# Optimization experiments

Measured on AMD Instinct MI355X. Metric: run time of the kernel, lower is better.

The kernel has to match this reference:

```python
import jax, jax.numpy as jnp
import numpy as np

NUM_CLASSES = 1000  # label vocabulary size (matches fill_max for label)
B = 16384
D_IN = 1024   # image_embedding
D_OUT = 256   # projection_dim


def setup_inputs() -> dict:
    key = jax.random.key(0)
    k = jax.random.split(key, 6)
    x = jax.random.normal(k[0], (B, D_IN), dtype=jnp.float32)
    label = jax.random.randint(k[1], (B,), 0, NUM_CLASSES, dtype=jnp.int64)
    scale = 1.0 / np.sqrt(D_IN)
    W1_w = jax.random.normal(k[2], (D_OUT, D_IN), dtype=jnp.float32) * scale
    W1_b = jax.random.normal(k[3], (D_OUT,), dtype=jnp.float32) * scale
    W2_w = jax.random.normal(k[4], (D_OUT, D_IN), dtype=jnp.float32) * scale
    W2_b = jax.random.normal(k[5], (D_OUT,), dtype=jnp.float32) * scale
    return {"x": x, "label": label, "W1_w": W1_w, "W1_b": W1_b,
            "W2_w": W2_w, "W2_b": W2_b}


def reference(x, label, W1_w, W1_b, W2_w, W2_b):
    # Leave-one-group-out mean, vectorized via segment sums.
    # Original: for each i, mean of x[label != label_i] (detached); zeros if none.
    b = x.shape[0]
    xd = jax.lax.stop_gradient(x)  # .detach() in the torch code
    label_sum = jax.ops.segment_sum(xd, label, num_segments=NUM_CLASSES)          # [C, D_IN]
    label_cnt = jax.ops.segment_sum(jnp.ones((b,), dtype=x.dtype), label,
                                    num_segments=NUM_CLASSES)                     # [C]
    total_sum = xd.sum(axis=0)                                                    # [D_IN]
    other_sum = total_sum[None, :] - label_sum[label]                             # [B, D_IN]
    other_cnt = jnp.asarray(b, x.dtype) - label_cnt[label]                        # [B]
    calculate_mean = jnp.where(other_cnt[:, None] > 0,
                               other_sum / jnp.maximum(other_cnt, 1)[:, None],
                               jnp.zeros((), x.dtype))                            # [B, D_IN]
    # W1(x) + W2(calculate_mean)  (torch Linear: y = x @ W.T + b)
    return x @ W1_w.T + W1_b + calculate_mean @ W2_w.T + W2_b
```

## Files before the change

### kernel.cpp

```cpp
#include <hip/hip_runtime.h>

constexpr int B      = 16384;
constexpr int D_IN   = 1024;
constexpr int D_OUT  = 256;
constexpr int NCLS   = 1000;

constexpr size_t OFF_XB  = 0;
constexpr size_t OFF_WB  = OFF_XB + (size_t)B * D_IN * 2;
constexpr size_t OFF_Y1  = OFF_WB + (size_t)512 * D_IN * 2;
constexpr size_t OFF_V   = OFF_Y1 + (size_t)B * D_OUT * 4;
constexpr size_t OFF_U   = OFF_V  + (size_t)1024 * D_OUT * 4;
constexpr size_t OFF_CNT = OFF_U  + 4096;

typedef short bf16x8 __attribute__((ext_vector_type(8)));
typedef float f32x4  __attribute__((ext_vector_type(4)));

__device__ __forceinline__ unsigned short f2bf(float f) {
    unsigned int u = __float_as_uint(f);
    return (unsigned short)((u + 0x7FFFu + ((u >> 16) & 1u)) >> 16);
}

__device__ __forceinline__ void cvt8(const float4& a, const float4& b, unsigned short* dst) {
    union { unsigned short u[8]; bf16x8 v; } r;
    r.u[0] = f2bf(a.x); r.u[1] = f2bf(a.y); r.u[2] = f2bf(a.z); r.u[3] = f2bf(a.w);
    r.u[4] = f2bf(b.x); r.u[5] = f2bf(b.y); r.u[6] = f2bf(b.z); r.u[7] = f2bf(b.w);
    *(bf16x8*)dst = r.v;
}

__device__ __forceinline__ void async16(const unsigned short* g, unsigned short* l) {
    __builtin_amdgcn_global_load_lds(
        (const __attribute__((address_space(1))) void*)g,
        (__attribute__((address_space(3))) void*)l,
        16, 0, 0);
}

constexpr int XCVT_BLKS = 8192;
constexpr int WCVT_BLKS = 256;
constexpr int VZ_BLKS   = 64;
__global__ __launch_bounds__(256)
void prep_kernel(const float* __restrict__ x,
                 const float* __restrict__ W1, const float* __restrict__ W2,
                 const int* __restrict__ label,
                 unsigned short* __restrict__ xb, unsigned short* __restrict__ Wb,
                 float* __restrict__ V, float* __restrict__ U, int* __restrict__ cnt) {
    const int blk = blockIdx.x, tid = threadIdx.x;
    if (blk < XCVT_BLKS) {
        size_t lin = (size_t)blk * 256 + tid;
        const float* src = x + lin * 8;
        float4 a = *(const float4*)src;
        float4 b = *(const float4*)(src + 4);
        cvt8(a, b, xb + lin * 8);
    } else if (blk < XCVT_BLKS + WCVT_BLKS) {
        int lin = (blk - XCVT_BLKS) * 256 + tid;
        int i = lin * 8;
        const float* src = (i < D_OUT * D_IN) ? (W1 + i) : (W2 + (i - D_OUT * D_IN));
        float4 a = *(const float4*)src;
        float4 b = *(const float4*)(src + 4);
        cvt8(a, b, Wb + i);
    } else if (blk < XCVT_BLKS + WCVT_BLKS + VZ_BLKS) {
        int lb = blk - (XCVT_BLKS + WCVT_BLKS);
        int base = (lb * 256 + tid) * 16;
#pragma unroll
        for (int q = 0; q < 4; ++q)
            *(float4*)(V + base + q * 4) = float4{0.f, 0.f, 0.f, 0.f};
        if (lb == 0 && tid < 64)
            *(float4*)(U + tid * 4) = float4{0.f, 0.f, 0.f, 0.f};
    } else {
        __shared__ int h[1024];
#pragma unroll
        for (int q = 0; q < 4; ++q) h[q * 256 + tid] = 0;
        __syncthreads();
        for (int r = 0; r < 64; ++r)
            atomicAdd(&h[label[r * 256 + tid]], 1);
        __syncthreads();
#pragma unroll
        for (int q = 0; q < 4; ++q) cnt[q * 256 + tid] = h[q * 256 + tid];
    }
}

__global__ __launch_bounds__(256)
void gemm_kernel(const unsigned short* __restrict__ xb,
                 const unsigned short* __restrict__ Wb,
                 const int* __restrict__ label,
                 float* __restrict__ y1,
                 float* __restrict__ V, float* __restrict__ U) {
    __shared__ unsigned short As[2][128][32];
    __shared__ unsigned short Bs[2][64][32];

    const int tid  = threadIdx.x;
    const int bid  = blockIdx.x;
    const int xcd   = bid & 7;
    const int local = bid >> 3;
    const int bx = xcd * 16 + (local & 15);
    const int by = local >> 4;
    const int bm = bx * 128;
    const int bn = by * 64;

    const int wave = tid >> 6, lane = tid & 63;
    const int quad = lane >> 4, l16 = lane & 15;
    const int wm = (wave >> 1) * 64;
    const int wn = (wave & 1) * 32;

    const unsigned short* aps[4];
#pragma unroll
    for (int rr = 0; rr < 4; ++rr) {
        int dd = rr * 256 + tid;
        int h = dd >> 9, r = (dd >> 2) & 127, c = dd & 3;
        aps[rr] = xb + (size_t)(bm + r) * D_IN + h * 32 + c * 8;
    }
    const unsigned short* bps[2];
#pragma unroll
    for (int rr = 0; rr < 2; ++rr) {
        int dd = rr * 256 + tid;
        int h = dd >> 8, r = (dd >> 2) & 63, c = dd & 3;
        bps[rr] = Wb + (size_t)(bn + r) * D_IN + h * 32 + c * 8;
    }

    f32x4 acc[4][2] = {};

    for (int k0 = 0; k0 < D_IN; k0 += 64) {
        __syncthreads();
#pragma unroll
        for (int rr = 0; rr < 4; ++rr)
            async16(aps[rr] + k0, &As[0][0][0] + rr * 2048 + wave * 512);
#pragma unroll
        for (int rr = 0; rr < 2; ++rr)
            async16(bps[rr] + k0, &Bs[0][0][0] + rr * 2048 + wave * 512);
        __syncthreads();

#pragma unroll
        for (int ks = 0; ks < 2; ++ks) {
            bf16x8 af[4], bfr[2];
#pragma unroll
            for (int i = 0; i < 4; ++i)
                af[i] = *(const bf16x8*)&As[ks][wm + i * 16 + l16][quad * 8];
#pragma unroll
            for (int j = 0; j < 2; ++j)
                bfr[j] = *(const bf16x8*)&Bs[ks][wn + j * 16 + l16][quad * 8];
#pragma unroll
            for (int i = 0; i < 4; ++i)
#pragma unroll
                for (int j = 0; j < 2; ++j)
                    acc[i][j] = __builtin_amdgcn_mfma_f32_16x16x32_bf16(af[i], bfr[j], acc[i][j], 0, 0, 0);
        }
    }

    if (by < 4) {
#pragma unroll
        for (int j = 0; j < 2; ++j) {
            const int n = bn + wn + j * 16 + l16;
#pragma unroll
            for (int i = 0; i < 4; ++i)
#pragma unroll
                for (int r = 0; r < 4; ++r) {
                    const int m = bm + wm + i * 16 + quad * 4 + r;
                    y1[(size_t)m * D_OUT + n] = acc[i][j][r];
                }
        }
    } else {
        int lab[4][4];
#pragma unroll
        for (int i = 0; i < 4; ++i)
#pragma unroll
            for (int r = 0; r < 4; ++r)
                lab[i][r] = label[bm + wm + i * 16 + quad * 4 + r] * D_OUT;

        const int nb = bn - 256;
#pragma unroll
        for (int j = 0; j < 2; ++j) {
            const int n = nb + wn + j * 16 + l16;
            float cs = 0.f;
#pragma unroll
            for (int i = 0; i < 4; ++i)
#pragma unroll
                for (int r = 0; r < 4; ++r) {
                    float v = acc[i][j][r];
                    cs += v;
                    atomicAdd(&V[lab[i][r] + n], v);
                }
            cs += __shfl_xor(cs, 16);
            cs += __shfl_xor(cs, 32);
            if (quad == 0) atomicAdd(&U[n], cs);
        }
    }
}

__global__ __launch_bounds__(256)
void epi_kernel(const float* __restrict__ y1, const float* __restrict__ V,
                const float* __restrict__ U,
                const float* __restrict__ b1, const float* __restrict__ b2,
                const int* __restrict__ cnt, const int* __restrict__ label,
                float* __restrict__ out) {
    const int tid = threadIdx.x;
    const int row = blockIdx.x * 64 + (tid >> 2);
    const int lab = label[row];
    const float inv = 1.0f / (float)(B - cnt[lab]);
    const float* yp = y1 + (size_t)row * D_OUT;
    const float* vp = V  + (size_t)lab * D_OUT;
    float* op = out + (size_t)row * D_OUT;
    const int c0 = (tid & 3) * 4;
#pragma unroll
    for (int it = 0; it < 16; ++it) {
        const int c = c0 + it * 16;
        float4 y = *(const float4*)(yp + c);
        float4 v = *(const float4*)(vp + c);
        float4 u = *(const float4*)(U + c);
        float4 a1 = *(const float4*)(b1 + c);
        float4 a2 = *(const float4*)(b2 + c);
        float4 o;
        o.x = y.x + a1.x + a2.x + (u.x - v.x) * inv;
        o.y = y.y + a1.y + a2.y + (u.y - v.y) * inv;
        o.z = y.z + a1.z + a2.z + (u.z - v.z) * inv;
        o.w = y.w + a1.w + a2.w + (u.w - v.w) * inv;
        *(float4*)(op + c) = o;
    }
}

extern "C" void kernel_launch(void* const* d_in, const int* in_sizes, int n_in,
                              void* d_out, int out_size, void* d_ws, size_t ws_size,
                              hipStream_t stream) {
    const float* x    = (const float*)d_in[0];
    const int*   lab  = (const int*)d_in[1];
    const float* W1_w = (const float*)d_in[2];
    const float* W1_b = (const float*)d_in[3];
    const float* W2_w = (const float*)d_in[4];
    const float* W2_b = (const float*)d_in[5];
    float* out = (float*)d_out;

    char* ws = (char*)d_ws;
    unsigned short* xb = (unsigned short*)(ws + OFF_XB);
    unsigned short* Wb = (unsigned short*)(ws + OFF_WB);
    float* y1 = (float*)(ws + OFF_Y1);
    float* V  = (float*)(ws + OFF_V);
    float* U  = (float*)(ws + OFF_U);
    int*   cnt = (int*)(ws + OFF_CNT);

    prep_kernel<<<XCVT_BLKS + WCVT_BLKS + VZ_BLKS + 1, 256, 0, stream>>>(
        x, W1_w, W2_w, lab, xb, Wb, V, U, cnt);
    gemm_kernel<<<1024, 256, 0, stream>>>(xb, Wb, lab, y1, V, U);
    epi_kernel<<<B / 64, 256, 0, stream>>>(y1, V, U, W1_b, W2_b, cnt, lab, out);
}
```

Baseline: 183.5 us.

## Enlarge GEMM tile to 128x128 with XOR-swizzled LDS and batch prep work

The GEMM block tile grows from 128x64 to 128x128, so each wave computes 64x64 and the grid halves to 512 blocks. This raises the MFMA-to-load ratio and cuts redundant reads of the x tiles. Shared memory is now a single 64-wide K slab per row with an XOR swizzle, intended to avoid LDS bank conflicts. The prep kernel converts 16 elements per thread, moves the label histogram to block 0 so it starts early, and batches its label loads. Costs are higher register use per thread (16 accumulators) and fewer blocks for 256 CUs, which may lower occupancy.

```diff
diff --git a/kernel.cpp b/kernel.cpp
--- a/kernel.cpp
+++ b/kernel.cpp
@@ -34,8 +34,8 @@
         16, 0, 0);
 }
 
-constexpr int XCVT_BLKS = 8192;
-constexpr int WCVT_BLKS = 256;
+constexpr int XCVT_BLKS = 4096;
+constexpr int WCVT_BLKS = 128;
 constexpr int VZ_BLKS   = 64;
 __global__ __launch_bounds__(256)
 void prep_kernel(const float* __restrict__ x,
@@ -44,37 +44,48 @@
                  unsigned short* __restrict__ xb, unsigned short* __restrict__ Wb,
                  float* __restrict__ V, float* __restrict__ U, int* __restrict__ cnt) {
     const int blk = blockIdx.x, tid = threadIdx.x;
-    if (blk < XCVT_BLKS) {
-        size_t lin = (size_t)blk * 256 + tid;
-        const float* src = x + lin * 8;
-        float4 a = *(const float4*)src;
-        float4 b = *(const float4*)(src + 4);
-        cvt8(a, b, xb + lin * 8);
-    } else if (blk < XCVT_BLKS + WCVT_BLKS) {
-        int lin = (blk - XCVT_BLKS) * 256 + tid;
-        int i = lin * 8;
+    if (blk == 0) {
+        __shared__ int h[1024];
+#pragma unroll
+        for (int q = 0; q < 4; ++q) h[q * 256 + tid] = 0;
+        __syncthreads();
+        for (int base = 0; base < 64; base += 16) {
+            int lv[16];
+#pragma unroll
+            for (int u = 0; u < 16; ++u) lv[u] = label[(base + u) * 256 + tid];
+#pragma unroll
+            for (int u = 0; u < 16; ++u) atomicAdd(&h[lv[u]], 1);
+        }
+        __syncthreads();
+#pragma unroll
+        for (int q = 0; q < 4; ++q) cnt[q * 256 + tid] = h[q * 256 + tid];
+    } else if (blk <= XCVT_BLKS) {
+        size_t lin = (size_t)(blk - 1) * 256 + tid;
+        const float* src = x + lin * 16;
+        float4 a0 = *(const float4*)(src);
+        float4 a1 = *(const float4*)(src + 4);
+        float4 a2 = *(const float4*)(src + 8);
+        float4 a3 = *(const float4*)(src + 12);
+        cvt8(a0, a1, xb + lin * 16);
+        cvt8(a2, a3, xb + lin * 16 + 8);
+    } else if (blk <= XCVT_BLKS + WCVT_BLKS) {
+        int lin = (blk - 1 - XCVT_BLKS) * 256 + tid;
+        int i = lin * 16;
         const float* src = (i < D_OUT * D_IN) ? (W1 + i) : (W2 + (i - D_OUT * D_IN));
-        float4 a = *(const float4*)src;
-        float4 b = *(const float4*)(src + 4);
-        cvt8(a, b, Wb + i);
-    } else if (blk < XCVT_BLKS + WCVT_BLKS + VZ_BLKS) {
-        int lb = blk - (XCVT_BLKS + WCVT_BLKS);
+        float4 a0 = *(const float4*)(src);
+        float4 a1 = *(const float4*)(src + 4);
+        float4 a2 = *(const float4*)(src + 8);
+        float4 a3 = *(const float4*)(src + 12);
+        cvt8(a0, a1, Wb + i);
+        cvt8(a2, a3, Wb + i + 8);
+    } else {
+        int lb = blk - 1 - XCVT_BLKS - WCVT_BLKS;
         int base = (lb * 256 + tid) * 16;
 #pragma unroll
         for (int q = 0; q < 4; ++q)
             *(float4*)(V + base + q * 4) = float4{0.f, 0.f, 0.f, 0.f};
         if (lb == 0 && tid < 64)
             *(float4*)(U + tid * 4) = float4{0.f, 0.f, 0.f, 0.f};
-    } else {
-        __shared__ int h[1024];
-#pragma unroll
-        for (int q = 0; q < 4; ++q) h[q * 256 + tid] = 0;
-        __syncthreads();
-        for (int r = 0; r < 64; ++r)
-            atomicAdd(&h[label[r * 256 + tid]], 1);
-        __syncthreads();
-#pragma unroll
-        for (int q = 0; q < 4; ++q) cnt[q * 256 + tid] = h[q * 256 + tid];
     }
 }
 
@@ -84,8 +95,8 @@
                  const int* __restrict__ label,
                  float* __restrict__ y1,
                  float* __restrict__ V, float* __restrict__ U) {
-    __shared__ unsigned short As[2][128][32];
-    __shared__ unsigned short Bs[2][64][32];
+    __shared__ unsigned short As[128][64];
+    __shared__ unsigned short Bs[128][64];
 
     const int tid  = threadIdx.x;
     const int bid  = blockIdx.x;
@@ -94,60 +105,58 @@
     const int bx = xcd * 16 + (local & 15);
     const int by = local >> 4;
     const int bm = bx * 128;
-    const int bn = by * 64;
+    const int bn = by * 128;
 
     const int wave = tid >> 6, lane = tid & 63;
     const int quad = lane >> 4, l16 = lane & 15;
     const int wm = (wave >> 1) * 64;
-    const int wn = (wave & 1) * 32;
+    const int wn = (wave & 1) * 64;
+    const int sx = l16 & 7;
 
     const unsigned short* aps[4];
+    const unsigned short* bps[4];
 #pragma unroll
     for (int rr = 0; rr < 4; ++rr) {
         int dd = rr * 256 + tid;
-        int h = dd >> 9, r = (dd >> 2) & 127, c = dd & 3;
-        aps[rr] = xb + (size_t)(bm + r) * D_IN + h * 32 + c * 8;
-    }
-    const unsigned short* bps[2];
-#pragma unroll
-    for (int rr = 0; rr < 2; ++rr) {
-        int dd = rr * 256 + tid;
-        int h = dd >> 8, r = (dd >> 2) & 63, c = dd & 3;
-        bps[rr] = Wb + (size_t)(bn + r) * D_IN + h * 32 + c * 8;
-    }
-
-    f32x4 acc[4][2] = {};
+        int r = dd >> 3, sl = dd & 7;
+        int sc = sl ^ (r & 7);
+        aps[rr] = xb + (size_t)(bm + r) * D_IN + sc * 8;
+        bps[rr] = Wb + (size_t)(bn + r) * D_IN + sc * 8;
+    }
+
+    f32x4 acc[4][4] = {};
 
     for (int k0 = 0; k0 < D_IN; k0 += 64) {
         __syncthreads();
 #pragma unroll
         for (int rr = 0; rr < 4; ++rr)
-            async16(aps[rr] + k0, &As[0][0][0] + rr * 2048 + wave * 512);
-#pragma unroll
-        for (int rr = 0; rr < 2; ++rr)
-            async16(bps[rr] + k0, &Bs[0][0][0] + rr * 2048 + wave * 512);
+            async16(aps[rr] + k0, &As[0][0] + rr * 2048 + wave * 512);
+#pragma unroll
+        for (int rr = 0; rr < 4; ++rr)
+            async16(bps[rr] + k0, &Bs[0][0] + rr * 2048 + wave * 512);
         __syncthreads();
 
 #pragma unroll
         for (int ks = 0; ks < 2; ++ks) {
-            bf16x8 af[4], bfr[2];
-#pragma unroll
-            for (int i = 0; i < 4; ++i)
-                af[i] = *(const bf16x8*)&As[ks][wm + i * 16 + l16][quad * 8];
-#pragma unroll
-            for (int j = 0; j < 2; ++j)
-                bfr[j] = *(const bf16x8*)&Bs[ks][wn + j * 16 + l16][quad * 8];
-#pragma unroll
-            for (int i = 0; i < 4; ++i)
-#pragma unroll
-                for (int j = 0; j < 2; ++j)
+            const int s = ks * 4 + quad;
+            bf16x8 af[4], bfr[4];
+#pragma unroll
+            for (int i = 0; i < 4; ++i)
+                af[i] = *(const bf16x8*)&As[wm + i * 16 + l16][((s ^ sx) * 8)];
+#pragma unroll
+            for (int j = 0; j < 4; ++j)
+                bfr[j] = *(const bf16x8*)&Bs[wn + j * 16 + l16][((s ^ sx) * 8)];
+#pragma unroll
+            for (int i = 0; i < 4; ++i)
+#pragma unroll
+                for (int j = 0; j < 4; ++j)
                     acc[i][j] = __builtin_amdgcn_mfma_f32_16x16x32_bf16(af[i], bfr[j], acc[i][j], 0, 0, 0);
         }
     }
 
-    if (by < 4) {
-#pragma unroll
-        for (int j = 0; j < 2; ++j) {
+    if (by < 2) {
+#pragma unroll
+        for (int j = 0; j < 4; ++j) {
             const int n = bn + wn + j * 16 + l16;
 #pragma unroll
             for (int i = 0; i < 4; ++i)
@@ -167,7 +176,7 @@
 
         const int nb = bn - 256;
 #pragma unroll
-        for (int j = 0; j < 2; ++j) {
+        for (int j = 0; j < 4; ++j) {
             const int n = nb + wn + j * 16 + l16;
             float cs = 0.f;
 #pragma unroll
@@ -235,8 +244,8 @@
     float* U  = (float*)(ws + OFF_U);
     int*   cnt = (int*)(ws + OFF_CNT);
 
-    prep_kernel<<<XCVT_BLKS + WCVT_BLKS + VZ_BLKS + 1, 256, 0, stream>>>(
+    prep_kernel<<<1 + XCVT_BLKS + WCVT_BLKS + VZ_BLKS, 256, 0, stream>>>(
         x, W1_w, W2_w, lab, xb, Wb, V, U, cnt);
-    gemm_kernel<<<1024, 256, 0, stream>>>(xb, Wb, lab, y1, V, U);
+    gemm_kernel<<<512, 256, 0, stream>>>(xb, Wb, lab, y1, V, U);
     epi_kernel<<<B / 64, 256, 0, stream>>>(y1, V, U, W1_b, W2_b, cnt, lab, out);
 }
```

New measurement: 160.1 us. 12.8% less time.
